# Performance work log

Hardware: AMD Instinct MI355X
Metric: run time of the kernel (lower is better)

Reference implementation:

```python
import jax, jax.numpy as jnp
import numpy as np

B, T, E, H = 2, 2048, 1024, 4
Dk = E // H          # 256 head qk dim
Dv = Dk * 2          # 512 head v dim (expansion_ratio=2)
EPS = 1e-5
ROPE_BASE = 10000.0


def setup_inputs() -> dict:
    key = jax.random.key(0)
    ks = jax.random.split(key, 7)
    s = 0.02  # small init matching xavier gains in reset_parameters
    return {
        "x": jax.random.normal(ks[0], (B, T, E), jnp.float32),
        "Wq": jax.random.normal(ks[1], (E, E), jnp.float32) * s,
        "Wk": jax.random.normal(ks[2], (E, E), jnp.float32) * s,
        "Wv": jax.random.normal(ks[3], (E, 2 * E), jnp.float32) * s,
        "Wg": jax.random.normal(ks[4], (E, 2 * E), jnp.float32) * s,
        "Wo": jax.random.normal(ks[5], (2 * E, E), jnp.float32) * s,
        "gn_weight": jnp.ones((Dv,), jnp.float32),
    }


def _rotary(q, k):
    # q,k: [b, t, h, d]; non-interleaved (GPT-NeoX) rotary over the full head dim
    d = q.shape[-1]
    inv_freq = 1.0 / (ROPE_BASE ** (jnp.arange(0, d, 2, dtype=jnp.float32) / d))
    t = jnp.arange(q.shape[1], dtype=jnp.float32)
    freqs = jnp.einsum('t,f->tf', t, inv_freq)      # [t, d/2]
    cos = jnp.cos(freqs)[None, :, None, :]
    sin = jnp.sin(freqs)[None, :, None, :]

    def rot(x):
        x1, x2 = x[..., : d // 2], x[..., d // 2:]
        return jnp.concatenate([x1 * cos - x2 * sin, x2 * cos + x1 * sin], axis=-1)

    return rot(q), rot(k)


def reference(x, Wq, Wk, Wv, Wg, Wo, gn_weight):
    b, t, e = x.shape
    q = (x @ Wq).reshape(b, t, H, Dk)
    k = (x @ Wk).reshape(b, t, H, Dk)
    q, k = _rotary(q, k)
    q = q.transpose(0, 2, 1, 3) * (Dk ** -0.5)      # [b,h,t,dk], scale = head_qk_dim^-0.5
    k = k.transpose(0, 2, 1, 3)
    v = (x @ Wv).reshape(b, t, H, Dv).transpose(0, 2, 1, 3)  # [b,h,t,dv]

    # RetNet per-head decay: gamma_h = 1 - 2^-(5+h)
    gamma = 1.0 - jnp.exp2(-5.0 - jnp.arange(H, dtype=jnp.float32))
    ti = jnp.arange(t)
    n = ti[:, None] - ti[None, :]                   # t - s
    decay = jnp.where(
        n >= 0,
        gamma[:, None, None] ** jnp.maximum(n, 0).astype(jnp.float32),
        0.0,
    )                                               # [h,t,t] causal decayed mask

    scores = jnp.einsum('bhtd,bhsd->bhts', q, k) * decay[None]
    o = jnp.einsum('bhts,bhsd->bhtd', scores, v)    # [b,h,t,dv]
    o = o.transpose(0, 2, 1, 3)                     # [b,t,h,dv]

    # per-head RMSNorm (group_norm over head_v_dim)
    rms = jnp.sqrt(jnp.mean(o * o, axis=-1, keepdims=True) + EPS)
    o = o / rms * gn_weight

    # NOTE: the given source multiplies by raw g_proj(x) (gate_fn not applied in forward)
    g = x @ Wg                                      # [b,t,2E]
    return (o.reshape(b, t, H * Dv) * g) @ Wo       # [b,t,E]
```

## Files before the change

kernel.cpp:

```cpp
#include <hip/hip_runtime.h>
#include <hip/hip_bf16.h>

#define B_ 2
#define T_ 2048
#define E_ 1024
#define DK 256
#define DV 512
#define MROWS 4096
#define LDQKVG 6144
#define CHK 128
#define NCHK 16

typedef __attribute__((ext_vector_type(8))) short short8;
typedef __attribute__((ext_vector_type(4))) short short4v;
typedef __attribute__((ext_vector_type(4))) float floatx4;

typedef __attribute__((address_space(3))) unsigned as3_u32;
typedef const __attribute__((address_space(1))) unsigned as1_u32;

static __device__ __forceinline__ void gld_lds16(const unsigned short* gsrc, unsigned short* ldst) {
  __builtin_amdgcn_global_load_lds((as1_u32*)gsrc, (as3_u32*)ldst, 16, 0, 0);
}

static __device__ __forceinline__ float bf2f(unsigned short u) {
  union { unsigned int i; float f; } x; x.i = ((unsigned int)u) << 16; return x.f;
}
static __device__ __forceinline__ unsigned short f2bf(float f) {
  __hip_bfloat16 h = __float2bfloat16(f);
  return __builtin_bit_cast(unsigned short, h);
}
static __device__ __forceinline__ float load_as_f(const float* p) { return *p; }
static __device__ __forceinline__ float load_as_f(const unsigned short* p) { return bf2f(*p); }

__global__ void __launch_bounds__(256) convx_kernel(const float* __restrict__ x,
                                                    unsigned short* __restrict__ xb) {
  int i = blockIdx.x * 256 + threadIdx.x;
  size_t base = (size_t)i * 8;
  float4 a = *(const float4*)(x + base);
  float4 b = *(const float4*)(x + base + 4);
  short8 o;
  o[0] = (short)f2bf(a.x); o[1] = (short)f2bf(a.y);
  o[2] = (short)f2bf(a.z); o[3] = (short)f2bf(a.w);
  o[4] = (short)f2bf(b.x); o[5] = (short)f2bf(b.y);
  o[6] = (short)f2bf(b.z); o[7] = (short)f2bf(b.w);
  *(short8*)(xb + base) = o;
}

template<typename TIN>
__global__ void __launch_bounds__(256) transpose_bf16_kernel(
    const TIN* __restrict__ in, int ldin, unsigned short* __restrict__ out, int ldout) {
  __shared__ float tile[32][33];
  int c0 = blockIdx.x * 32, r0 = blockIdx.y * 32;
  int tx = threadIdx.x & 31, ty = threadIdx.x >> 5;
#pragma unroll
  for (int i = 0; i < 32; i += 8)
    tile[ty + i][tx] = load_as_f(&in[(size_t)(r0 + ty + i) * ldin + c0 + tx]);
  __syncthreads();
#pragma unroll
  for (int i = 0; i < 32; i += 8)
    out[(size_t)(c0 + ty + i) * ldout + r0 + tx] = f2bf(tile[tx][ty + i]);
}

__global__ void __launch_bounds__(256) transpose_weights_kernel(
    const float* __restrict__ Wq, const float* __restrict__ Wk,
    const float* __restrict__ Wv, const float* __restrict__ Wg,
    unsigned short* __restrict__ out) {
  __shared__ float tile[32][33];
  int bid = blockIdx.x;
  const float* in; unsigned short* o; int ldin, nbx;
  if (bid < 1024)      { in = Wq; o = out;                       ldin = 1024; nbx = 32; }
  else if (bid < 2048) { in = Wk; o = out + (size_t)1024 * 1024; ldin = 1024; nbx = 32; bid -= 1024; }
  else if (bid < 4096) { in = Wv; o = out + (size_t)2048 * 1024; ldin = 2048; nbx = 64; bid -= 2048; }
  else                 { in = Wg; o = out + (size_t)4096 * 1024; ldin = 2048; nbx = 64; bid -= 4096; }
  int c0 = (bid % nbx) * 32, r0 = (bid / nbx) * 32;
  int tx = threadIdx.x & 31, ty = threadIdx.x >> 5;
#pragma unroll
  for (int i = 0; i < 32; i += 8)
    tile[ty + i][tx] = in[(size_t)(r0 + ty + i) * ldin + c0 + tx];
  __syncthreads();
#pragma unroll
  for (int i = 0; i < 32; i += 8)
    o[(size_t)(c0 + ty + i) * 1024 + r0 + tx] = f2bf(tile[tx][ty + i]);
}

__global__ void __launch_bounds__(256) kts_transpose_kernel(
    const unsigned short* __restrict__ in, unsigned short* __restrict__ out) {
  __shared__ float tile[32][33];
  int c0 = blockIdx.x * 32, r0 = blockIdx.y * 32;
  int tx = threadIdx.x & 31, ty = threadIdx.x >> 5;
#pragma unroll
  for (int i = 0; i < 32; i += 8)
    tile[ty + i][tx] = bf2f(in[(size_t)(r0 + ty + i) * LDQKVG + c0 + tx]);
  __syncthreads();
  int h = c0 >> 8;
  float lg = log2f(1.0f - exp2f(-5.0f - (float)h));
  int t = r0 + tx;
  float fac = exp2f((float)(CHK - (t & (CHK - 1))) * lg);
#pragma unroll
  for (int i = 0; i < 32; i += 8)
    out[(size_t)(c0 + ty + i) * MROWS + r0 + tx] = f2bf(tile[tx][ty + i] * fac);
}

template<int BM, int BN, int KK, bool F32OUT>
__global__ void __launch_bounds__(512, 4) gemm3_kernel(
    const unsigned short* __restrict__ A, int lda,
    const unsigned short* __restrict__ Bt, int ldb,
    void* __restrict__ Cp, int ldc, int ccol0) {
  constexpr int NT = KK / 32;
  constexpr int AG = BM / 128;
  constexpr int BG = BN / 128;
  __shared__ __align__(16) unsigned short lds[3][(BM + BN) * 32];
  const int tid = threadIdx.x;
  const int lane = tid & 63;
  const int wid = tid >> 6;
  const int wm = wid >> 2, wn = wid & 3;
  const int m0 = blockIdx.x * BM;
  const int n0 = blockIdx.y * BN;
  const unsigned short* Ab = A + (size_t)m0 * lda;
  const unsigned short* Bb = Bt + (size_t)n0 * ldb;

  auto stage = [&](int sl, int t) {
    const int k0 = t * 32;
#pragma unroll
    for (int j = 0; j < AG; ++j) {
      int g = wid * AG + j;
      int ci = g * 64 + lane;
      int row = ci >> 2, c = ci & 3;
      int cs = c ^ ((row >> 1) & 3);
      gld_lds16(Ab + (size_t)row * lda + k0 + cs * 8, &lds[sl][g * 512]);
    }
#pragma unroll
    for (int j = 0; j < BG; ++j) {
      int g = wid * BG + j;
      int ci = g * 64 + lane;
      int row = ci >> 2, c = ci & 3;
      int cs = c ^ ((row >> 1) & 3);
      gld_lds16(Bb + (size_t)row * ldb + k0 + cs * 8, &lds[sl][BM * 32 + g * 512]);
    }
  };

  floatx4 acc[4][4];
#pragma unroll
  for (int i = 0; i < 4; i++)
#pragma unroll
    for (int j = 0; j < 4; j++)
      acc[i][j] = (floatx4){0.f, 0.f, 0.f, 0.f};

  stage(0, 0);
  stage(1, 1);

  int cur = 0;
#pragma unroll 1
  for (int t = 0; t < NT; ++t) {
    if (t + 1 < NT) {
      if constexpr (AG + BG == 3) asm volatile("s_waitcnt vmcnt(3)" ::: "memory");
      else if constexpr (AG + BG == 2) asm volatile("s_waitcnt vmcnt(2)" ::: "memory");
      else asm volatile("s_waitcnt vmcnt(4)" ::: "memory");
    } else {
      asm volatile("s_waitcnt vmcnt(0)" ::: "memory");
    }
    __builtin_amdgcn_s_barrier();
    asm volatile("" ::: "memory");
    int sl = cur + 2; if (sl >= 3) sl -= 3;
    if (t + 2 < NT) stage(sl, t + 2);

    const unsigned short* As_ = lds[cur];
    const unsigned short* Bs_ = lds[cur] + BM * 32;
    short8 af[4], bfv[4];
#pragma unroll
    for (int i = 0; i < 4; ++i) {
      int row = wm * 64 + i * 16 + (lane & 15);
      af[i] = *(const short8*)&As_[row * 32 + (((lane >> 4) ^ ((row >> 1) & 3)) * 8)];
      int nn = wn * 64 + i * 16 + (lane & 15);
      bfv[i] = *(const short8*)&Bs_[nn * 32 + (((lane >> 4) ^ ((nn >> 1) & 3)) * 8)];
    }
#pragma unroll
    for (int i = 0; i < 4; ++i)
#pragma unroll
      for (int j = 0; j < 4; ++j)
        acc[i][j] = __builtin_amdgcn_mfma_f32_16x16x32_bf16(af[i], bfv[j], acc[i][j], 0, 0, 0);
    cur = cur + 1 == 3 ? 0 : cur + 1;
  }

#pragma unroll
  for (int i = 0; i < 4; ++i)
#pragma unroll
    for (int j = 0; j < 4; ++j)
#pragma unroll
      for (int r = 0; r < 4; ++r) {
        int row = m0 + wm * 64 + i * 16 + (lane >> 4) * 4 + r;
        int col = ccol0 + n0 + wn * 64 + j * 16 + (lane & 15);
        float v = acc[i][j][r];
        if (F32OUT) ((float*)Cp)[(size_t)row * ldc + col] = v;
        else ((unsigned short*)Cp)[(size_t)row * ldc + col] = f2bf(v);
      }
}

template<int MTILE, bool F32OUT>
static __device__ __forceinline__ void gemm_tile(
    const unsigned short* __restrict__ A, int lda,
    const unsigned short* __restrict__ Bt, int ldb,
    int K, char* __restrict__ Cbase, int ldc) {
  __shared__ unsigned short As[MTILE * 32];
  __shared__ unsigned short Bs[128 * 32];
  constexpr int MB = MTILE / 32;
  constexpr int AJ = MTILE / 64;
  const int tid = threadIdx.x;
  const int lane = tid & 63;
  const int wid = tid >> 6;
  const int wr = (wid >> 1) * (MTILE / 2), wc = (wid & 1) * 64;
  floatx4 acc[MB][4];
#pragma unroll
  for (int i = 0; i < MB; i++)
#pragma unroll
    for (int j = 0; j < 4; j++)
      acc[i][j] = (floatx4){0.f, 0.f, 0.f, 0.f};

  for (int k0 = 0; k0 < K; k0 += 32) {
    __syncthreads();
#pragma unroll
    for (int j = 0; j < AJ; ++j) {
      int ci = (wid * AJ + j) * 64 + lane;
      int row = ci >> 2, cc = (ci & 3) * 8;
      gld_lds16(&A[(size_t)row * lda + k0 + cc], &As[(wid * AJ + j) * 512]);
    }
#pragma unroll
    for (int j = 0; j < 2; ++j) {
      int ci = (wid * 2 + j) * 64 + lane;
      int row = ci >> 2, cc = (ci & 3) * 8;
      gld_lds16(&Bt[(size_t)row * ldb + k0 + cc], &Bs[(wid * 2 + j) * 512]);
    }
    __syncthreads();
    short8 af[MB], bfr[4];
#pragma unroll
    for (int mb = 0; mb < MB; mb++)
      af[mb] = *(const short8*)&As[(wr + mb * 16 + (lane & 15)) * 32 + (lane >> 4) * 8];
#pragma unroll
    for (int nb = 0; nb < 4; nb++)
      bfr[nb] = *(const short8*)&Bs[(wc + nb * 16 + (lane & 15)) * 32 + (lane >> 4) * 8];
#pragma unroll
    for (int mb = 0; mb < MB; mb++)
#pragma unroll
      for (int nb = 0; nb < 4; nb++)
        acc[mb][nb] = __builtin_amdgcn_mfma_f32_16x16x32_bf16(af[mb], bfr[nb], acc[mb][nb], 0, 0, 0);
  }
#pragma unroll
  for (int mb = 0; mb < MB; mb++)
#pragma unroll
    for (int nb = 0; nb < 4; nb++)
#pragma unroll
      for (int r = 0; r < 4; r++) {
        int row = wr + mb * 16 + (lane >> 4) * 4 + r;
        int col = wc + nb * 16 + (lane & 15);
        float v = acc[mb][nb][r];
        if (F32OUT) ((float*)Cbase)[(size_t)row * ldc + col] = v;
        else ((unsigned short*)Cbase)[(size_t)row * ldc + col] = f2bf(v);
      }
}

template<int MTILE, bool F32OUT>
__global__ void __launch_bounds__(256) gemm_bt_kernel(
    const unsigned short* __restrict__ A, int lda,
    const unsigned short* __restrict__ Bt, int ldb, int K,
    void* __restrict__ Cp, int ldc, int ccol0) {
  size_t m0 = (size_t)blockIdx.x * MTILE;
  size_t n0 = (size_t)blockIdx.y * 128;
  size_t esz = F32OUT ? 4 : 2;
  gemm_tile<MTILE, F32OUT>(A + m0 * lda, lda, Bt + n0 * ldb, ldb, K,
                           (char*)Cp + esz * (m0 * ldc + ccol0 + n0), ldc);
}

__global__ void __launch_bounds__(256) rope_kernel(unsigned short* __restrict__ qkvg) {
  int idx = blockIdx.x * 256 + threadIdx.x;
  int j = idx & 127;
  int h = (idx >> 7) & 3;
  int row = idx >> 9;
  int t = row & (T_ - 1);
  float invf = exp2f(-(float)j * (13.287712379549449f / 128.0f));
  float ang = (float)t * invf;
  float c = cosf(ang), s = sinf(ang);
  float lg = log2f(1.0f - exp2f(-5.0f - (float)h));
  float sq = 0.0625f * exp2f((float)(t & (CHK - 1)) * lg);
  size_t base = (size_t)row * LDQKVG + h * DK + j;
  float q1 = bf2f(qkvg[base]), q2 = bf2f(qkvg[base + 128]);
  float k1 = bf2f(qkvg[base + E_]), k2 = bf2f(qkvg[base + E_ + 128]);
  qkvg[base]            = f2bf((q1 * c - q2 * s) * sq);
  qkvg[base + 128]      = f2bf((q2 * c + q1 * s) * sq);
  qkvg[base + E_]       = f2bf(k1 * c - k2 * s);
  qkvg[base + E_ + 128] = f2bf(k2 * c + k1 * s);
}

__global__ void __launch_bounds__(256) state_kernel(
    const unsigned short* __restrict__ kTs, const unsigned short* __restrict__ vT,
    unsigned short* __restrict__ Sbuf) {
  const int lane = threadIdx.x & 63, wid = threadIdx.x >> 6;
  const int bh = blockIdx.x & 7, dkt = (blockIdx.x >> 3) & 3, dvt = (blockIdx.x >> 5) & 15;
  const int b = bh >> 2, h = bh & 3;
  const float lg = log2f(1.0f - exp2f(-5.0f - (float)h));
  const float g128 = exp2f((float)CHK * lg);
  const int dk0 = dkt * 64 + wid * 16;
  const int dv0 = dvt * 32;
  const unsigned short* arow = kTs + (size_t)(h * DK + dk0 + (lane & 15)) * MROWS + b * T_ + (lane >> 4) * 8;
  const unsigned short* brow = vT + (size_t)(h * DV + dv0 + (lane & 15)) * MROWS + b * T_ + (lane >> 4) * 8;
  floatx4 acc[2];
  acc[0] = (floatx4){0.f, 0.f, 0.f, 0.f};
  acc[1] = (floatx4){0.f, 0.f, 0.f, 0.f};
#pragma unroll 1
  for (int c = 0; c < NCHK; ++c) {
    size_t sb = (size_t)(c * 8 + bh) * (DV * DK);
#pragma unroll
    for (int nb = 0; nb < 2; ++nb) {
      short4v o;
#pragma unroll
      for (int r = 0; r < 4; ++r) o[r] = (short)f2bf(acc[nb][r]);
      *(short4v*)&Sbuf[sb + (size_t)(dv0 + nb * 16 + (lane & 15)) * DK + dk0 + (lane >> 4) * 4] = o;
    }
#pragma unroll
    for (int nb = 0; nb < 2; ++nb)
#pragma unroll
      for (int r = 0; r < 4; ++r) acc[nb][r] *= g128;
#pragma unroll
    for (int ks = 0; ks < 4; ++ks) {
      short8 a = *(const short8*)(arow + c * CHK + ks * 32);
#pragma unroll
      for (int nb = 0; nb < 2; ++nb) {
        short8 bb = *(const short8*)(brow + (size_t)nb * 16 * MROWS + c * CHK + ks * 32);
        acc[nb] = __builtin_amdgcn_mfma_f32_16x16x32_bf16(a, bb, acc[nb], 0, 0, 0);
      }
    }
  }
}

__global__ void __launch_bounds__(256) retention2_kernel(
    const unsigned short* __restrict__ qkvg, const unsigned short* __restrict__ vT,
    const unsigned short* __restrict__ Sbuf, const float* __restrict__ gnw,
    unsigned short* __restrict__ og, float* __restrict__ ssbuf) {
  __shared__ unsigned short k_lds[2][32 * 256];
  __shared__ unsigned short v_lds[2][256 * 32];
  __shared__ unsigned short s_lds[4][16 * 40];
  const int tid = threadIdx.x, lane = tid & 63, wid = tid >> 6;
  const int bh  = blockIdx.x & 7;
  const int c   = (blockIdx.x >> 3) & 15;
  const int dvh = (blockIdx.x >> 7) & 1;
  const int rhf = (blockIdx.x >> 8) & 1;
  const int b = bh >> 2, h = bh & 3;
  const float lg = log2f(1.0f - exp2f(-5.0f - (float)h));
  const int rb0 = b * T_ + c * CHK + rhf * 64;
  const int taub = rhf * 64 + wid * 16;
  const int nst = rhf ? 4 : 2;
  const unsigned short* kbase = qkvg + (size_t)(b * T_ + c * CHK) * LDQKVG + E_ + h * DK;
  const unsigned short* vbase = vT + (size_t)(h * DV + dvh * 256) * MROWS + b * T_ + c * CHK;
  const unsigned short* Sp = Sbuf + (size_t)(c * 8 + bh) * (DV * DK) + (size_t)dvh * 256 * DK;

  auto stage = [&](int buf, int st) {
    int s0 = st * 32;
#pragma unroll
    for (int j = 0; j < 4; ++j) {
      int ci = (wid * 4 + j) * 64 + lane;
      int row = ci >> 5, cc = ci & 31;
      int cs = cc ^ (row & 7);
      gld_lds16(kbase + (size_t)(s0 + row) * LDQKVG + cs * 8, &k_lds[buf][(wid * 4 + j) * 512]);
    }
#pragma unroll
    for (int j = 0; j < 4; ++j) {
      int ci = (wid * 4 + j) * 64 + lane;
      int dv = ci >> 2, cc = ci & 3;
      int cs = cc ^ ((dv ^ (dv >> 2)) & 3);
      gld_lds16(vbase + (size_t)dv * MROWS + s0 + cs * 8, &v_lds[buf][(wid * 4 + j) * 512]);
    }
  };

  stage(0, 0);

  short8 qf[8];
  {
    int qrow = rb0 + wid * 16 + (lane & 15);
    const unsigned short* qp = qkvg + (size_t)qrow * LDQKVG + h * DK + (lane >> 4) * 8;
#pragma unroll
    for (int kk = 0; kk < 8; kk++) qf[kk] = *(const short8*)(qp + kk * 32);
  }
  floatx4 oacc[16];
#pragma unroll
  for (int nb = 0; nb < 16; ++nb) oacc[nb] = (floatx4){0.f, 0.f, 0.f, 0.f};
#pragma unroll
  for (int ks = 0; ks < 8; ++ks) {
#pragma unroll
    for (int nb = 0; nb < 16; ++nb) {
      short8 sf = *(const short8*)&Sp[(size_t)(nb * 16 + (lane & 15)) * DK + ks * 32 + (lane >> 4) * 8];
      oacc[nb] = __builtin_amdgcn_mfma_f32_16x16x32_bf16(qf[ks], sf, oacc[nb], 0, 0, 0);
    }
  }

#pragma unroll 1
  for (int st = 0; st < nst; ++st) {
    const int cur = st & 1;
    __syncthreads();
    if (st + 1 < nst) stage(cur ^ 1, st + 1);
#pragma unroll
    for (int ch = 0; ch < 2; ++ch) {
      floatx4 f = (floatx4){0.f, 0.f, 0.f, 0.f};
      const int srow = ch * 16 + (lane & 15);
#pragma unroll
      for (int kk = 0; kk < 8; kk++) {
        int cc = (kk * 4 + (lane >> 4)) ^ (srow & 7);
        short8 kf = *(const short8*)&k_lds[cur][srow * 256 + cc * 8];
        f = __builtin_amdgcn_mfma_f32_16x16x32_bf16(qf[kk], kf, f, 0, 0, 0);
      }
#pragma unroll
      for (int r = 0; r < 4; ++r) {
        int lr = (lane >> 4) * 4 + r;
        int sig = st * 32 + ch * 16 + (lane & 15);
        int n = taub + lr - sig;
        float val = (n >= 0) ? f[r] * exp2f(-(float)sig * lg) : 0.0f;
        s_lds[wid][lr * 40 + ch * 16 + (lane & 15)] = f2bf(val);
      }
    }
    short8 af = *(const short8*)&s_lds[wid][(lane & 15) * 40 + (lane >> 4) * 8];
#pragma unroll
    for (int nb = 0; nb < 16; ++nb) {
      int dv = nb * 16 + (lane & 15);
      int cc = (lane >> 4) ^ ((dv ^ (dv >> 2)) & 3);
      short8 vf = *(const short8*)&v_lds[cur][dv * 32 + cc * 8];
      oacc[nb] = __builtin_amdgcn_mfma_f32_16x16x32_bf16(af, vf, oacc[nb], 0, 0, 0);
    }
  }
#pragma unroll
  for (int r = 0; r < 4; ++r) {
    float ss = 0.f;
#pragma unroll
    for (int nb = 0; nb < 16; nb++) { float xv = oacc[nb][r]; ss += xv * xv; }
    ss += __shfl_xor(ss, 1, 64);
    ss += __shfl_xor(ss, 2, 64);
    ss += __shfl_xor(ss, 4, 64);
    ss += __shfl_xor(ss, 8, 64);
    if ((lane & 15) == 0) {
      int row = rb0 + wid * 16 + (lane >> 4) * 4 + r;
      ssbuf[(size_t)row * 8 + h * 2 + dvh] = ss;
    }
  }
#pragma unroll
  for (int r = 0; r < 4; ++r) {
    int row = rb0 + wid * 16 + (lane >> 4) * 4 + r;
    size_t growbase = (size_t)row * LDQKVG + 4096 + h * DV + dvh * 256;
    size_t orowbase = (size_t)row * LDQKVG + h * DV + dvh * 256;
#pragma unroll
    for (int nb = 0; nb < 16; nb++) {
      int col = nb * 16 + (lane & 15);
      float gv = bf2f(qkvg[growbase + col]);
      og[orowbase + col] = f2bf(oacc[nb][r] * gnw[dvh * 256 + col] * gv);
    }
  }
}

__global__ void __launch_bounds__(256) normalize_kernel(
    unsigned short* __restrict__ og, const float* __restrict__ ssbuf) {
  int i = blockIdx.x * 256 + threadIdx.x;
  size_t e0 = (size_t)i * 8;
  int row = (int)(e0 >> 11);
  int col = (int)(e0 & 2047);
  int h = col >> 9;
  float ss = ssbuf[(size_t)row * 8 + h * 2] + ssbuf[(size_t)row * 8 + h * 2 + 1];
  float inv = rsqrtf(ss * (1.0f / 512.0f) + 1e-5f);
  size_t a = (size_t)row * LDQKVG + col;
  short8 v = *(const short8*)(og + a);
#pragma unroll
  for (int j = 0; j < 8; j++) v[j] = (short)f2bf(bf2f((unsigned short)v[j]) * inv);
  *(short8*)(og + a) = v;
}

extern "C" void kernel_launch(void* const* d_in, const int* in_sizes, int n_in,
                              void* d_out, int out_size, void* d_ws, size_t ws_size,
                              hipStream_t stream) {
  const float* x   = (const float*)d_in[0];
  const float* Wq  = (const float*)d_in[1];
  const float* Wk  = (const float*)d_in[2];
  const float* Wv  = (const float*)d_in[3];
  const float* Wg  = (const float*)d_in[4];
  const float* Wo  = (const float*)d_in[5];
  const float* gnw = (const float*)d_in[6];
  float* out = (float*)d_out;

  char* ws = (char*)d_ws;
  size_t off = 0;
  auto alloc = [&](size_t bytes) { char* p = ws + off; off += (bytes + 255) & ~(size_t)255; return p; };
  unsigned short* qkvg = (unsigned short*)alloc((size_t)MROWS * LDQKVG * 2);
  unsigned short* vT   = (unsigned short*)alloc((size_t)2048 * MROWS * 2);
  char* regS = alloc((size_t)NCHK * 8 * DV * DK * 2);
  unsigned short* Sbuf  = (unsigned short*)regS;
  unsigned short* xb    = (unsigned short*)regS;
  unsigned short* WallT = (unsigned short*)(regS + 8388608);
  char* regK = alloc((size_t)1024 * MROWS * 2);
  unsigned short* kTs = (unsigned short*)regK;
  unsigned short* WoT = (unsigned short*)regK;
  float* ssbuf = (float*)alloc((size_t)MROWS * 8 * 4);
  unsigned short* og = qkvg + 2048;

  convx_kernel<<<2048, 256, 0, stream>>>(x, xb);

  transpose_weights_kernel<<<6144, 256, 0, stream>>>(Wq, Wk, Wv, Wg, WallT);

  gemm3_kernel<128, 256, 1024, false><<<dim3(32, 24), 512, 0, stream>>>(
      xb, 1024, WallT, 1024, qkvg, LDQKVG, 0);

  rope_kernel<<<8192, 256, 0, stream>>>(qkvg);

  kts_transpose_kernel<<<dim3(32, 128), 256, 0, stream>>>(qkvg + E_, kTs);

  transpose_bf16_kernel<unsigned short><<<dim3(64, 128), 256, 0, stream>>>(qkvg + 2048, LDQKVG, vT, MROWS);

  state_kernel<<<512, 256, 0, stream>>>(kTs, vT, Sbuf);

  transpose_bf16_kernel<float><<<dim3(32, 64), 256, 0, stream>>>(Wo, 1024, WoT, 2048);

  retention2_kernel<<<512, 256, 0, stream>>>(qkvg, vT, Sbuf, gnw, og, ssbuf);

  normalize_kernel<<<4096, 256, 0, stream>>>(og, ssbuf);

  gemm_bt_kernel<64, true><<<dim3(64, 8), 256, 0, stream>>>(og, LDQKVG, WoT, 2048, 2048, out, E_, 0);
}
```

Baseline: 237.3 us.

## Generalize pipelined GEMM and use it for QKVG and output projections

Turns the triple-buffered LDS GEMM into a template with configurable warp layout and occupancy. It adds an XCD-aware block-index swizzle that groups neighbouring tiles on the same chiplet. The QKVG projection now runs on 4 waves with 128x256 tiles (each wave covers 128x64), which raises per-wave register pressure. The output projection drops the simple double-sync gemm_bt kernel for the pipelined one with 128x128 tiles, which gives only 256 blocks and may underfill the GPU.

```diff
diff --git a/kernel.cpp b/kernel.cpp
--- a/kernel.cpp
+++ b/kernel.cpp
@@ -101,23 +101,29 @@
     out[(size_t)(c0 + ty + i) * MROWS + r0 + tx] = f2bf(tile[tx][ty + i] * fac);
 }
 
-template<int BM, int BN, int KK, bool F32OUT>
-__global__ void __launch_bounds__(512, 4) gemm3_kernel(
+template<int BM, int BN, int WM_W, int WN_W, int MINW, bool F32OUT>
+__global__ void __launch_bounds__(WM_W * WN_W * 64, MINW) gemmp_kernel(
     const unsigned short* __restrict__ A, int lda,
-    const unsigned short* __restrict__ Bt, int ldb,
-    void* __restrict__ Cp, int ldc, int ccol0) {
-  constexpr int NT = KK / 32;
-  constexpr int AG = BM / 128;
-  constexpr int BG = BN / 128;
+    const unsigned short* __restrict__ Bt, int ldb, int K,
+    void* __restrict__ Cp, int ldc, int ccol0, int nbx) {
+  constexpr int WAVES = WM_W * WN_W;
+  constexpr int AG = BM / 16 / WAVES;
+  constexpr int BG = BN / 16 / WAVES;
+  constexpr int RM = BM / WM_W;
+  constexpr int CN = BN / WN_W;
+  constexpr int MB = RM / 16, NB = CN / 16;
   __shared__ __align__(16) unsigned short lds[3][(BM + BN) * 32];
   const int tid = threadIdx.x;
   const int lane = tid & 63;
   const int wid = tid >> 6;
-  const int wm = wid >> 2, wn = wid & 3;
-  const int m0 = blockIdx.x * BM;
-  const int n0 = blockIdx.y * BN;
+  const int wm = wid / WN_W, wn = wid % WN_W;
+  const int q8 = gridDim.x >> 3;
+  const int bid = (blockIdx.x & 7) * q8 + (blockIdx.x >> 3);
+  const int m0 = (bid % nbx) * BM;
+  const int n0 = (bid / nbx) * BN;
   const unsigned short* Ab = A + (size_t)m0 * lda;
   const unsigned short* Bb = Bt + (size_t)n0 * ldb;
+  const int NT = K / 32;
 
   auto stage = [&](int sl, int t) {
     const int k0 = t * 32;
@@ -139,11 +145,11 @@
     }
   };
 
-  floatx4 acc[4][4];
-#pragma unroll
-  for (int i = 0; i < 4; i++)
-#pragma unroll
-    for (int j = 0; j < 4; j++)
+  floatx4 acc[MB][NB];
+#pragma unroll
+  for (int i = 0; i < MB; i++)
+#pragma unroll
+    for (int j = 0; j < NB; j++)
       acc[i][j] = (floatx4){0.f, 0.f, 0.f, 0.f};
 
   stage(0, 0);
@@ -153,9 +159,11 @@
 #pragma unroll 1
   for (int t = 0; t < NT; ++t) {
     if (t + 1 < NT) {
-      if constexpr (AG + BG == 3) asm volatile("s_waitcnt vmcnt(3)" ::: "memory");
-      else if constexpr (AG + BG == 2) asm volatile("s_waitcnt vmcnt(2)" ::: "memory");
-      else asm volatile("s_waitcnt vmcnt(4)" ::: "memory");
+      if constexpr (AG + BG == 2) asm volatile("s_waitcnt vmcnt(2)" ::: "memory");
+      else if constexpr (AG + BG == 3) asm volatile("s_waitcnt vmcnt(3)" ::: "memory");
+      else if constexpr (AG + BG == 4) asm volatile("s_waitcnt vmcnt(4)" ::: "memory");
+      else if constexpr (AG + BG == 6) asm volatile("s_waitcnt vmcnt(6)" ::: "memory");
+      else asm volatile("s_waitcnt vmcnt(8)" ::: "memory");
     } else {
       asm volatile("s_waitcnt vmcnt(0)" ::: "memory");
     }
@@ -166,108 +174,37 @@
 
     const unsigned short* As_ = lds[cur];
     const unsigned short* Bs_ = lds[cur] + BM * 32;
-    short8 af[4], bfv[4];
-#pragma unroll
-    for (int i = 0; i < 4; ++i) {
-      int row = wm * 64 + i * 16 + (lane & 15);
+    short8 af[MB], bfv[NB];
+#pragma unroll
+    for (int i = 0; i < MB; ++i) {
+      int row = wm * RM + i * 16 + (lane & 15);
       af[i] = *(const short8*)&As_[row * 32 + (((lane >> 4) ^ ((row >> 1) & 3)) * 8)];
-      int nn = wn * 64 + i * 16 + (lane & 15);
-      bfv[i] = *(const short8*)&Bs_[nn * 32 + (((lane >> 4) ^ ((nn >> 1) & 3)) * 8)];
-    }
-#pragma unroll
-    for (int i = 0; i < 4; ++i)
-#pragma unroll
-      for (int j = 0; j < 4; ++j)
+    }
+#pragma unroll
+    for (int j = 0; j < NB; ++j) {
+      int nn = wn * CN + j * 16 + (lane & 15);
+      bfv[j] = *(const short8*)&Bs_[nn * 32 + (((lane >> 4) ^ ((nn >> 1) & 3)) * 8)];
+    }
+#pragma unroll
+    for (int i = 0; i < MB; ++i)
+#pragma unroll
+      for (int j = 0; j < NB; ++j)
         acc[i][j] = __builtin_amdgcn_mfma_f32_16x16x32_bf16(af[i], bfv[j], acc[i][j], 0, 0, 0);
     cur = cur + 1 == 3 ? 0 : cur + 1;
   }
 
 #pragma unroll
-  for (int i = 0; i < 4; ++i)
-#pragma unroll
-    for (int j = 0; j < 4; ++j)
+  for (int i = 0; i < MB; ++i)
+#pragma unroll
+    for (int j = 0; j < NB; ++j)
 #pragma unroll
       for (int r = 0; r < 4; ++r) {
-        int row = m0 + wm * 64 + i * 16 + (lane >> 4) * 4 + r;
-        int col = ccol0 + n0 + wn * 64 + j * 16 + (lane & 15);
+        int row = m0 + wm * RM + i * 16 + (lane >> 4) * 4 + r;
+        int col = ccol0 + n0 + wn * CN + j * 16 + (lane & 15);
         float v = acc[i][j][r];
         if (F32OUT) ((float*)Cp)[(size_t)row * ldc + col] = v;
         else ((unsigned short*)Cp)[(size_t)row * ldc + col] = f2bf(v);
       }
-}
-
-template<int MTILE, bool F32OUT>
-static __device__ __forceinline__ void gemm_tile(
-    const unsigned short* __restrict__ A, int lda,
-    const unsigned short* __restrict__ Bt, int ldb,
-    int K, char* __restrict__ Cbase, int ldc) {
-  __shared__ unsigned short As[MTILE * 32];
-  __shared__ unsigned short Bs[128 * 32];
-  constexpr int MB = MTILE / 32;
-  constexpr int AJ = MTILE / 64;
-  const int tid = threadIdx.x;
-  const int lane = tid & 63;
-  const int wid = tid >> 6;
-  const int wr = (wid >> 1) * (MTILE / 2), wc = (wid & 1) * 64;
-  floatx4 acc[MB][4];
-#pragma unroll
-  for (int i = 0; i < MB; i++)
-#pragma unroll
-    for (int j = 0; j < 4; j++)
-      acc[i][j] = (floatx4){0.f, 0.f, 0.f, 0.f};
-
-  for (int k0 = 0; k0 < K; k0 += 32) {
-    __syncthreads();
-#pragma unroll
-    for (int j = 0; j < AJ; ++j) {
-      int ci = (wid * AJ + j) * 64 + lane;
-      int row = ci >> 2, cc = (ci & 3) * 8;
-      gld_lds16(&A[(size_t)row * lda + k0 + cc], &As[(wid * AJ + j) * 512]);
-    }
-#pragma unroll
-    for (int j = 0; j < 2; ++j) {
-      int ci = (wid * 2 + j) * 64 + lane;
-      int row = ci >> 2, cc = (ci & 3) * 8;
-      gld_lds16(&Bt[(size_t)row * ldb + k0 + cc], &Bs[(wid * 2 + j) * 512]);
-    }
-    __syncthreads();
-    short8 af[MB], bfr[4];
-#pragma unroll
-    for (int mb = 0; mb < MB; mb++)
-      af[mb] = *(const short8*)&As[(wr + mb * 16 + (lane & 15)) * 32 + (lane >> 4) * 8];
-#pragma unroll
-    for (int nb = 0; nb < 4; nb++)
-      bfr[nb] = *(const short8*)&Bs[(wc + nb * 16 + (lane & 15)) * 32 + (lane >> 4) * 8];
-#pragma unroll
-    for (int mb = 0; mb < MB; mb++)
-#pragma unroll
-      for (int nb = 0; nb < 4; nb++)
-        acc[mb][nb] = __builtin_amdgcn_mfma_f32_16x16x32_bf16(af[mb], bfr[nb], acc[mb][nb], 0, 0, 0);
-  }
-#pragma unroll
-  for (int mb = 0; mb < MB; mb++)
-#pragma unroll
-    for (int nb = 0; nb < 4; nb++)
-#pragma unroll
-      for (int r = 0; r < 4; r++) {
-        int row = wr + mb * 16 + (lane >> 4) * 4 + r;
-        int col = wc + nb * 16 + (lane & 15);
-        float v = acc[mb][nb][r];
-        if (F32OUT) ((float*)Cbase)[(size_t)row * ldc + col] = v;
-        else ((unsigned short*)Cbase)[(size_t)row * ldc + col] = f2bf(v);
-      }
-}
-
-template<int MTILE, bool F32OUT>
-__global__ void __launch_bounds__(256) gemm_bt_kernel(
-    const unsigned short* __restrict__ A, int lda,
-    const unsigned short* __restrict__ Bt, int ldb, int K,
-    void* __restrict__ Cp, int ldc, int ccol0) {
-  size_t m0 = (size_t)blockIdx.x * MTILE;
-  size_t n0 = (size_t)blockIdx.y * 128;
-  size_t esz = F32OUT ? 4 : 2;
-  gemm_tile<MTILE, F32OUT>(A + m0 * lda, lda, Bt + n0 * ldb, ldb, K,
-                           (char*)Cp + esz * (m0 * ldc + ccol0 + n0), ldc);
 }
 
 __global__ void __launch_bounds__(256) rope_kernel(unsigned short* __restrict__ qkvg) {
@@ -499,8 +436,8 @@
 
   transpose_weights_kernel<<<6144, 256, 0, stream>>>(Wq, Wk, Wv, Wg, WallT);
 
-  gemm3_kernel<128, 256, 1024, false><<<dim3(32, 24), 512, 0, stream>>>(
-      xb, 1024, WallT, 1024, qkvg, LDQKVG, 0);
+  gemmp_kernel<128, 256, 1, 4, 2, false><<<768, 256, 0, stream>>>(
+      xb, 1024, WallT, 1024, 1024, qkvg, LDQKVG, 0, 32);
 
   rope_kernel<<<8192, 256, 0, stream>>>(qkvg);
 
@@ -516,5 +453,6 @@
 
   normalize_kernel<<<4096, 256, 0, stream>>>(og, ssbuf);
 
-  gemm_bt_kernel<64, true><<<dim3(64, 8), 256, 0, stream>>>(og, LDQKVG, WoT, 2048, 2048, out, E_, 0);
-}
+  gemmp_kernel<128, 128, 2, 2, 3, true><<<256, 256, 0, stream>>>(
+      og, LDQKVG, WoT, 2048, 2048, out, E_, 0, 32);
+}
```

New measurement: 226.8 us. 1.05x faster.
